# Optimization experiments

Measured on AMD Instinct MI355X. Metric: run time of the kernel, lower is better.

Reference implementation:

```python
import jax, jax.numpy as jnp
import numpy as np


def _silu(x):
    return x * jax.nn.sigmoid(x)


def _ln(x, w, b, eps=1e-5):
    mu = x.mean(-1, keepdims=True)
    xc = x - mu
    var = (xc * xc).mean(-1, keepdims=True)
    return xc * jax.lax.rsqrt(var + eps) * w + b


def _segsum(a):
    # a: (..., Q) -> (..., Q, Q) lower-triangular cumulative segment sums
    Q = a.shape[-1]
    cs = jnp.cumsum(a, axis=-1)
    ss = cs[..., :, None] - cs[..., None, :]
    mask = jnp.tril(jnp.ones((Q, Q), dtype=bool))
    return jnp.where(mask, ss, -jnp.inf)


def _ssd(x, A, Bm, Cm, chunk=64):
    # Mamba2 SSD dual (chunked) form. x:(b,l,h,p) pre-scaled by dt, A:(b,l,h)=dt*A, Bm/Cm:(b,l,n)
    b, l, h, p = x.shape
    c = l // chunk
    x = x.reshape(b, c, chunk, h, p)
    A = A.reshape(b, c, chunk, h).transpose(0, 3, 1, 2)          # (b,h,c,q)
    Bm = Bm.reshape(b, c, chunk, -1)
    Cm = Cm.reshape(b, c, chunk, -1)
    Acs = jnp.cumsum(A, axis=-1)                                  # (b,h,c,q)
    Lmat = jnp.exp(_segsum(A))                                    # (b,h,c,q,q)
    Yd = jnp.einsum('bcln,bcsn,bhcls,bcshp->bclhp', Cm, Bm, Lmat, x)
    dec = jnp.exp(Acs[..., -1:] - Acs)                            # (b,h,c,q)
    states = jnp.einsum('bcln,bhcl,bclhp->bchpn', Bm, dec, x)     # (b,c,h,p,n)
    cdec = jnp.exp(Acs[..., -1]).transpose(2, 0, 1)               # (c,b,h)
    st = states.transpose(1, 0, 2, 3, 4)                          # (c,b,h,p,n)

    def step(carry, inp):
        s, d = inp
        return carry * d[..., None, None] + s, carry

    _, prev = jax.lax.scan(step, jnp.zeros_like(st[0]), (st, cdec))
    prev = prev.transpose(1, 0, 2, 3, 4)                          # (b,c,h,p,n)
    Yo = jnp.einsum('bcln,bchpn,bhcl->bclhp', Cm, prev, jnp.exp(Acs))
    return (Yd + Yo).reshape(b, l, h, p)


def _mamba(x, in_w, in_b, conv_w, conv_b, A_log, D, dt_bias, rms_w, out_w, headdim, d_state):
    b, l, _ = x.shape
    nh = A_log.shape[0]
    di = nh * headdim
    zxbcdt = x @ in_w.T + in_b
    z = zxbcdt[..., :di]
    xBC = zxbcdt[..., di:2 * di + 2 * d_state]
    dt = jax.nn.softplus(zxbcdt[..., -nh:] + dt_bias)             # (b,l,nh)
    K = conv_w.shape[-1]
    xp = jnp.pad(xBC, ((0, 0), (K - 1, 0), (0, 0)))               # causal depthwise conv
    xBC = sum(xp[:, k:k + l, :] * conv_w[:, k] for k in range(K))
    xBC = _silu(xBC + conv_b)
    xs = xBC[..., :di].reshape(b, l, nh, headdim)
    Bm = xBC[..., di:di + d_state]
    Cm = xBC[..., di + d_state:]
    A = -jnp.exp(A_log)
    y = _ssd(xs * dt[..., None], dt * A, Bm, Cm)
    y = y + D[None, None, :, None] * xs
    y = y.reshape(b, l, di) * _silu(z)                            # gated RMSNorm
    y = y * jax.lax.rsqrt(jnp.mean(y * y, -1, keepdims=True) + 1e-5) * rms_w
    return y @ out_w.T


def setup_inputs() -> dict:
    key = jax.random.key(0)
    ks = iter(jax.random.split(key, 64))

    def nrm(shape, s):
        return jax.random.normal(next(ks), shape, jnp.float32) * s

    d = {}
    d['x'] = jax.random.normal(next(ks), (4, 128, 64, 64), jnp.float32)
    d['seed_tok_w'] = nrm((8, 128), 0.08)
    d['seed_tok_b'] = jnp.zeros((8,), jnp.float32)
    d['seed_detok_w'] = nrm((128, 8), 0.3)
    d['seed_detok_b'] = jnp.zeros((128,), jnp.float32)
    d['sm_in_w'] = nrm((66, 8), 0.3)
    d['sm_in_b'] = jnp.zeros((66,), jnp.float32)
    d['sm_conv_w'] = nrm((48, 3), 0.3)
    d['sm_conv_b'] = jnp.zeros((48,), jnp.float32)
    d['sm_A_log'] = jnp.log(jnp.arange(1, 3, dtype=jnp.float32))
    d['sm_D'] = jnp.ones((2,), jnp.float32)
    d['sm_dt_bias'] = jnp.full((2,), -4.0, jnp.float32)
    d['sm_rms_w'] = jnp.ones((16,), jnp.float32)
    d['sm_out_w'] = nrm((8, 16), 0.2)
    d['cm_in_w'] = nrm((2, 196, 16), 0.2)
    d['cm_in_b'] = jnp.zeros((2, 196), jnp.float32)
    d['cm_conv_w'] = nrm((2, 160, 3), 0.3)
    d['cm_conv_b'] = jnp.zeros((2, 160), jnp.float32)
    d['cm_A_log'] = jnp.tile(jnp.log(jnp.arange(1, 5, dtype=jnp.float32)), (2, 1))
    d['cm_D'] = jnp.ones((2, 4), jnp.float32)
    d['cm_dt_bias'] = jnp.full((2, 4), -4.0, jnp.float32)
    d['cm_rms_w'] = jnp.ones((2, 32), jnp.float32)
    d['cm_out_w'] = nrm((2, 16, 32), 0.15)
    d['cross_W'] = jnp.eye(8, dtype=jnp.float32) + 0.01 * jax.random.normal(next(ks), (8, 8), jnp.float32)
    d['norm1_w'] = jnp.ones((128,), jnp.float32)
    d['norm1_b'] = jnp.zeros((128,), jnp.float32)
    d['norm2_w'] = jnp.ones((128,), jnp.float32)
    d['norm2_b'] = jnp.zeros((128,), jnp.float32)
    d['fc1_w'] = nrm((256, 128), 0.08)
    d['fc1_b'] = jnp.zeros((256,), jnp.float32)
    d['dw_w'] = nrm((256, 1, 3, 3), 0.2)
    d['dw_b'] = jnp.zeros((256,), jnp.float32)
    d['fc2_w'] = nrm((128, 256), 0.06)
    d['fc2_b'] = jnp.zeros((128,), jnp.float32)
    d['skip_scale'] = jnp.ones((1,), jnp.float32)
    return d


def reference(x, seed_tok_w, seed_tok_b, seed_detok_w, seed_detok_b,
              sm_in_w, sm_in_b, sm_conv_w, sm_conv_b, sm_A_log, sm_D, sm_dt_bias, sm_rms_w, sm_out_w,
              cm_in_w, cm_in_b, cm_conv_w, cm_conv_b, cm_A_log, cm_D, cm_dt_bias, cm_rms_w, cm_out_w,
              cross_W, norm1_w, norm1_b, norm2_w, norm2_b,
              fc1_w, fc1_b, dw_w, dw_b, fc2_w, fc2_b, skip_scale):
    B, C, H, W = x.shape
    L = H * W
    # --- GlobalSeed ---
    g = jnp.einsum('bchw,gc->bghw', x, seed_tok_w) + seed_tok_b[None, :, None, None]
    gf = g.reshape(B, -1, L).transpose(0, 2, 1)                   # (B,L,G)
    gf = _mamba(gf, sm_in_w, sm_in_b, sm_conv_w, sm_conv_b, sm_A_log, sm_D,
                sm_dt_bias, sm_rms_w, sm_out_w, 8, 16) + gf
    det = jnp.einsum('blg,cg->blc', gf, seed_detok_w) + seed_detok_b
    seed = x + det.transpose(0, 2, 1).reshape(B, C, H, W)
    # --- split-channel cascaded SSD (shared weights across splits) ---
    xn = _ln(x.reshape(B, C, L).transpose(0, 2, 1), norm1_w, norm1_b)   # (B,L,C)
    S = cross_W.shape[0]
    xs = jnp.stack(jnp.split(xn, S, axis=-1))                     # (S,B,L,C/S)

    def cascade(xi):
        for i in range(cm_in_w.shape[0]):
            xi = _mamba(xi, cm_in_w[i], cm_in_b[i], cm_conv_w[i], cm_conv_b[i],
                        cm_A_log[i], cm_D[i], cm_dt_bias[i], cm_rms_w[i], cm_out_w[i], 8, 64)
        return xi

    ys = jax.vmap(cascade)(xs) + xs * skip_scale
    # --- SubCrossToken mixing ---
    gm = ys.mean(axis=2)                                          # (S,B,Cs)
    wsm = jax.nn.softmax(cross_W, axis=1)
    gmix = jnp.einsum('qbc,qp->pbc', gm, wsm)
    ys = ys + gmix[:, :, None, :]
    out = ys.transpose(1, 2, 0, 3).reshape(B, L, -1)
    out = _ln(out, norm2_w, norm2_b)
    out = out.transpose(0, 2, 1).reshape(B, C, H, W) + seed
    # --- ConvFFN ---
    h1 = jnp.einsum('bchw,oc->bohw', out, fc1_w) + fc1_b[None, :, None, None]
    dw = jax.lax.conv_general_dilated(h1, dw_w, (1, 1), 'SAME',
                                      feature_group_count=h1.shape[1],
                                      dimension_numbers=('NCHW', 'OIHW', 'NCHW'))
    h2 = jax.nn.gelu(dw + dw_b[None, :, None, None])
    ffn = jnp.einsum('bohw,co->bchw', h2, fc2_w) + fc2_b[None, :, None, None]
    return out + ffn
```

## Files before the change

### kernel.cpp

```cpp
#include <hip/hip_runtime.h>
#include <math.h>

#define B_ 4
#define CCH 128
#define HH 64
#define WW 64
#define LL 4096
#define NCHK 64

__device__ __forceinline__ float siluf(float x) { return x / (1.f + __expf(-x)); }
__device__ __forceinline__ float softplusf(float x) { return (x > 20.f) ? x : log1pf(__expf(x)); }
__device__ __forceinline__ int swz(int n, int l) {
  return (n << 6) + ((((l >> 2) ^ ((n >> 2) & 15)) << 2) | (l & 3));
}

__global__ __launch_bounds__(256) void k_seedtok(const float* __restrict__ x,
    const float* __restrict__ w, const float* __restrict__ bias, float* __restrict__ gf)
{
  __shared__ float tile[128*65];
  __shared__ float sw[8*128];
  __shared__ float bl[8];
  int tid = threadIdx.x;
  int b = blockIdx.x >> 6;
  int l0 = (blockIdx.x & 63) << 6;
  for (int i = tid; i < 1024; i += 256) sw[i] = w[i];
  if (tid < 8) bl[tid] = bias[tid];
  for (int i = tid; i < 8192; i += 256) {
    int l = i & 63, c = i >> 6;
    tile[c*65 + l] = x[((size_t)b*CCH + c)*LL + l0 + l];
  }
  __syncthreads();
  int l = tid & 63, q = tid >> 6;
  float a0 = bl[2*q], a1 = bl[2*q+1];
  const float* w0 = &sw[(2*q)*128];
  const float* w1 = &sw[(2*q+1)*128];
#pragma unroll 4
  for (int c = 0; c < 128; ++c) {
    float xv = tile[c*65 + l];
    a0 += xv * w0[c];
    a1 += xv * w1[c];
  }
  *(float2*)&gf[((size_t)b*LL + l0 + l)*8 + 2*q] = make_float2(a0, a1);
}

template<int DIN, int NZ, int NDS, int NDT>
__global__ __launch_bounds__(256) void k_inproj(
    const float* __restrict__ src, int srcMode,
    const float* __restrict__ in_w, const float* __restrict__ in_b,
    const float* __restrict__ conv_w, const float* __restrict__ conv_b,
    const float* __restrict__ dt_bias,
    float* __restrict__ zb, float* __restrict__ dtb,
    float* __restrict__ xsb, float* __restrict__ Bb, float* __restrict__ Cb)
{
  constexpr int NXBC = NZ + 2*NDS;
  constexpr int NTOT = 2*NZ + 2*NDS + NDT;
  constexpr int NZQ  = NZ/4;
  constexpr int NDSQ = NDS/4;
  constexpr int XP   = DIN + 1;
  __shared__ float xt[66*XP];
  __shared__ float wl[NTOT*DIN];
  __shared__ float cwl[NXBC*3];
  __shared__ float cbl[NXBC];
  __shared__ float ibl[NTOT];
  __shared__ float dts[64*NDT];
  __shared__ float hp[NXBC*2];
  int tid = threadIdx.x;
  int seq = blockIdx.x >> 6;
  int l0  = (blockIdx.x & 63) << 6;
  for (int i = tid; i < NTOT*DIN; i += 256) wl[i] = in_w[i];
  for (int i = tid; i < NXBC*3; i += 256) cwl[i] = conv_w[i];
  for (int i = tid; i < NXBC; i += 256) cbl[i] = conv_b[i];
  for (int i = tid; i < NTOT; i += 256) ibl[i] = in_b[i];
  const float* sp; int sstr;
  if (srcMode == 0) { sp = src + (size_t)seq*LL*DIN; sstr = DIN; }
  else { sp = src + (size_t)(seq & 3)*LL*CCH + (seq >> 2)*16; sstr = CCH; }
  for (int i = tid; i < 66*DIN; i += 256) {
    int r = i / DIN, d = i % DIN;
    int l = l0 - 2 + r;
    xt[r*XP + d] = (l >= 0) ? sp[(size_t)l*sstr + d] : 0.f;
  }
  __syncthreads();
  for (int i = tid; i < 2*NXBC; i += 256) {
    int t = i & 1, ch = i >> 1;
    const float* wr = &wl[(NZ + ch)*DIN];
    const float* xp = &xt[t*XP];
    float acc = 0.f;
#pragma unroll
    for (int d = 0; d < DIN; ++d) acc += xp[d]*wr[d];
    hp[ch*2 + t] = acc;
  }
  __syncthreads();
  int l = tid & 63, w4 = tid >> 6;
  float xr2[DIN];
#pragma unroll
  for (int d = 0; d < DIN; ++d) xr2[d] = xt[(l+2)*XP + d];
  size_t gl = (size_t)seq*LL + l0 + l;
  int tok = l0 + l;
  float v0ok = (tok >= 2) ? 1.f : 0.f;
  float v1ok = (tok >= 1) ? 1.f : 0.f;
  {
    float zv[NZQ];
#pragma unroll
    for (int j = 0; j < NZQ; ++j) {
      int row = w4*NZQ + j;
      const float* wr = &wl[row*DIN];
      float acc = ibl[row];
#pragma unroll
      for (int d = 0; d < DIN; ++d) acc += xr2[d]*wr[d];
      zv[j] = acc;
    }
#pragma unroll
    for (int g = 0; g < NZQ/4; ++g)
      *(float4*)&zb[gl*NZ + w4*NZQ + 4*g] = make_float4(zv[4*g], zv[4*g+1], zv[4*g+2], zv[4*g+3]);
  }
  if (w4 < NDT) {
    int row = NTOT - NDT + w4;
    const float* wr = &wl[row*DIN];
    float acc = ibl[row] + dt_bias[w4];
#pragma unroll
    for (int d = 0; d < DIN; ++d) acc += xr2[d]*wr[d];
    dts[l*NDT + w4] = softplusf(acc);
  }
  auto convch = [&](int ch) -> float {
    int row = NZ + ch;
    const float* wr = &wl[row*DIN];
    float pm = 0.f;
#pragma unroll
    for (int d = 0; d < DIN; ++d) pm += xr2[d]*wr[d];
    float m1 = __shfl_up(pm, 1, 64);
    float m2 = __shfl_up(pm, 2, 64);
    float h0 = hp[ch*2 + 0], h1 = hp[ch*2 + 1];
    if (l == 0) m1 = h1;
    m2 = (l == 0) ? h0 : ((l == 1) ? h1 : m2);
    float ib = ibl[row];
    float conv = cbl[ch] + (m2+ib)*v0ok*cwl[ch*3+0] + (m1+ib)*v1ok*cwl[ch*3+1] + (pm+ib)*cwl[ch*3+2];
    return siluf(conv);
  };
  {
    float xv[NZQ];
#pragma unroll
    for (int j = 0; j < NZQ; ++j) xv[j] = convch(w4*NZQ + j);
#pragma unroll
    for (int g = 0; g < NZQ/4; ++g)
      *(float4*)&xsb[gl*NZ + w4*NZQ + 4*g] = make_float4(xv[4*g], xv[4*g+1], xv[4*g+2], xv[4*g+3]);
  }
  {
    float bv[NDSQ];
#pragma unroll
    for (int j = 0; j < NDSQ; ++j) bv[j] = convch(NZ + w4*NDSQ + j);
#pragma unroll
    for (int g = 0; g < NDSQ/4; ++g)
      *(float4*)&Bb[gl*NDS + w4*NDSQ + 4*g] = make_float4(bv[4*g], bv[4*g+1], bv[4*g+2], bv[4*g+3]);
  }
  {
    float cv[NDSQ];
#pragma unroll
    for (int j = 0; j < NDSQ; ++j) cv[j] = convch(NZ + NDS + w4*NDSQ + j);
#pragma unroll
    for (int g = 0; g < NDSQ/4; ++g)
      *(float4*)&Cb[gl*NDS + w4*NDSQ + 4*g] = make_float4(cv[4*g], cv[4*g+1], cv[4*g+2], cv[4*g+3]);
  }
  __syncthreads();
  if (tid < 64) {
    if constexpr (NDT == 4) {
      *(float4*)&dtb[((size_t)seq*LL + l0 + tid)*4] =
          make_float4(dts[tid*4], dts[tid*4+1], dts[tid*4+2], dts[tid*4+3]);
    } else {
      *(float2*)&dtb[((size_t)seq*LL + l0 + tid)*NDT] = make_float2(dts[tid*NDT], dts[tid*NDT+1]);
    }
  }
}

__global__ __launch_bounds__(256, 3) void k_inssd(
    const float* __restrict__ src, int srcMode,
    const float* __restrict__ in_w, const float* __restrict__ in_b,
    const float* __restrict__ conv_w, const float* __restrict__ conv_b,
    const float* __restrict__ dt_bias, const float* __restrict__ A_log,
    float* __restrict__ zb, float* __restrict__ xsb, float* __restrict__ Cb,
    float* __restrict__ ybuf, float* __restrict__ states,
    float* __restrict__ cdec, float* __restrict__ acsOut)
{
  const int DIN = 16, NZ = 32, NDS = 64, DI = 32;
  const int NXBC = 160, NTOT = 196;
  __shared__ float sm[12518];
  float* Bt  = sm;
  float* Ct  = sm + 4096;
  float* U   = sm + 8192;
  float* wl  = U;
  float* cwl = U + 3136;
  float* cbl = U + 3616;
  float* ibl = U + 3776;
  float* hp  = U + 3972;
  float* ha  = U + 4292;
  float* xde = U;
  int tid = threadIdx.x;
  int cid = blockIdx.x & 63;
  int seq = blockIdx.x >> 6;
  int l0  = cid << 6;
  int lane = tid & 63, w = tid >> 6;
  const float* sp; int sstr;
  if (srcMode == 0) { sp = src + (size_t)seq*LL*DIN; sstr = DIN; }
  else { sp = src + (size_t)(seq & 3)*LL*CCH + (seq >> 2)*16; sstr = CCH; }
  float xr2[DIN];
  {
    const float* p = sp + (size_t)(l0 + lane)*sstr;
#pragma unroll
    for (int k = 0; k < 4; ++k) {
      float4 v = *(const float4*)(p + 4*k);
      xr2[4*k+0]=v.x; xr2[4*k+1]=v.y; xr2[4*k+2]=v.z; xr2[4*k+3]=v.w;
    }
  }
  for (int i = tid; i < NTOT*DIN; i += 256) wl[i] = in_w[i];
  for (int i = tid; i < NXBC*3; i += 256) cwl[i] = conv_w[i];
  for (int i = tid; i < NXBC; i += 256) cbl[i] = conv_b[i];
  for (int i = tid; i < NTOT; i += 256) ibl[i] = in_b[i];
  if (tid < 32) {
    int t = tid >> 4, d = tid & 15;
    int tok = l0 - 2 + t;
    ha[t*17 + d] = (tok >= 0) ? sp[(size_t)tok*sstr + d] : 0.f;
  }
  __syncthreads();
  for (int i = tid; i < 2*NXBC; i += 256) {
    int t = i & 1, ch = i >> 1;
    const float* wr = &wl[(NZ + ch)*DIN];
    const float* hr = &ha[t*17];
    float acc = 0.f;
#pragma unroll
    for (int d = 0; d < DIN; ++d) acc += hr[d]*wr[d];
    hp[ch*2 + t] = acc;
  }
  __syncthreads();
  size_t gl = (size_t)seq*LL + l0 + lane;
  int tok = l0 + lane;
  float v0ok = (tok >= 2) ? 1.f : 0.f;
  float v1ok = (tok >= 1) ? 1.f : 0.f;
  {
    float zv[8];
#pragma unroll
    for (int j = 0; j < 8; ++j) {
      int row = w*8 + j;
      const float* wr = &wl[row*DIN];
      float acc = ibl[row];
#pragma unroll
      for (int d = 0; d < DIN; ++d) acc += xr2[d]*wr[d];
      zv[j] = acc;
    }
    *(float4*)&zb[gl*NZ + w*8 + 0] = make_float4(zv[0], zv[1], zv[2], zv[3]);
    *(float4*)&zb[gl*NZ + w*8 + 4] = make_float4(zv[4], zv[5], zv[6], zv[7]);
  }
  float dtv;
  {
    int row = NTOT - 4 + w;
    const float* wr = &wl[row*DIN];
    float acc = ibl[row] + dt_bias[w];
#pragma unroll
    for (int d = 0; d < DIN; ++d) acc += xr2[d]*wr[d];
    dtv = softplusf(acc);
  }
  auto convch = [&](int ch) -> float {
    int row = NZ + ch;
    const float* wr = &wl[row*DIN];
    float pm = 0.f;
#pragma unroll
    for (int d = 0; d < DIN; ++d) pm += xr2[d]*wr[d];
    float m1 = __shfl_up(pm, 1, 64);
    float m2 = __shfl_up(pm, 2, 64);
    float h0 = hp[ch*2 + 0], h1 = hp[ch*2 + 1];
    if (lane == 0) m1 = h1;
    m2 = (lane == 0) ? h0 : ((lane == 1) ? h1 : m2);
    float ib = ibl[row];
    float conv = cbl[ch] + (m2+ib)*v0ok*cwl[ch*3+0] + (m1+ib)*v1ok*cwl[ch*3+1] + (pm+ib)*cwl[ch*3+2];
    return siluf(conv);
  };
  float xv[8];
#pragma unroll
  for (int j = 0; j < 8; ++j) xv[j] = convch(w*8 + j);
  *(float4*)&xsb[gl*DI + w*8 + 0] = make_float4(xv[0], xv[1], xv[2], xv[3]);
  *(float4*)&xsb[gl*DI + w*8 + 4] = make_float4(xv[4], xv[5], xv[6], xv[7]);
#pragma unroll
  for (int j = 0; j < 16; ++j) {
    int n = w*16 + j;
    Bt[swz(n, lane)] = convch(NZ + n);
  }
  {
    float cv[16];
#pragma unroll
    for (int j = 0; j < 16; ++j) {
      int n = w*16 + j;
      cv[j] = convch(NZ + NDS + n);
      Ct[swz(n, lane)] = cv[j];
    }
#pragma unroll
    for (int g = 0; g < 4; ++g)
      *(float4*)&Cb[gl*NDS + w*16 + 4*g] = make_float4(cv[4*g], cv[4*g+1], cv[4*g+2], cv[4*g+3]);
  }
  __syncthreads();
  float Aval = -__expf(A_log[w]);
  float v = dtv * Aval;
#pragma unroll
  for (int off = 1; off < 64; off <<= 1) {
    float t = __shfl_up(v, off, 64);
    if (lane >= off) v += t;
  }
  float acs_l = v;
  float m = __shfl(v, 31, 64);
  float acsLast = __shfl(v, 63, 64);
  float el = __expf(fminf(acs_l - m, 60.f));
  float fl = __expf(fminf(m - acs_l, 60.f));
  {
    float s1 = dtv*fl;
    float* xe = &xde[(w*64 + lane)*8];
    *(float4*)xe     = make_float4(xv[0]*s1, xv[1]*s1, xv[2]*s1, xv[3]*s1);
    *(float4*)(xe+4) = make_float4(xv[4]*s1, xv[5]*s1, xv[6]*s1, xv[7]*s1);
  }
  int lt = (tid >> 4) << 2, st = (tid & 15) << 2;
  float acc[4][4] = {};
#pragma unroll 4
  for (int n = 0; n < 64; ++n) {
    float4 cvv = *(const float4*)&Ct[swz(n, lt)];
    float4 bvv = *(const float4*)&Bt[swz(n, st)];
    float cc[4] = {cvv.x, cvv.y, cvv.z, cvv.w};
    float bb[4] = {bvv.x, bvv.y, bvv.z, bvv.w};
#pragma unroll
    for (int i2 = 0; i2 < 4; ++i2)
#pragma unroll
      for (int j2 = 0; j2 < 4; ++j2)
        acc[i2][j2] += cc[i2]*bb[j2];
  }
  __syncthreads();
#pragma unroll
  for (int j = 0; j < 4; ++j) {
    *(float4*)&Ct[swz(st + j, lt)] = make_float4(acc[0][j], acc[1][j], acc[2][j], acc[3][j]);
  }
  __syncthreads();
  int lg = lane >> 2, lm = lane & 3;
  float ya[8] = {0,0,0,0,0,0,0,0};
#pragma unroll 4
  for (int s = 0; s < 64; ++s) {
    float g = Ct[(s << 6) + (((lg ^ ((s >> 2) & 15))) << 2 | lm)];
    g = (s <= lane) ? g : 0.f;
    const float* xr = &xde[(w*64 + s)*8];
    float4 a0 = *(const float4*)xr, a1 = *(const float4*)(xr + 4);
    ya[0] += g*a0.x; ya[1] += g*a0.y; ya[2] += g*a0.z; ya[3] += g*a0.w;
    ya[4] += g*a1.x; ya[5] += g*a1.y; ya[6] += g*a1.z; ya[7] += g*a1.w;
  }
  float* yp = &ybuf[gl*DI + w*8];
  *(float4*)yp     = make_float4(ya[0]*el, ya[1]*el, ya[2]*el, ya[3]*el);
  *(float4*)(yp+4) = make_float4(ya[4]*el, ya[5]*el, ya[6]*el, ya[7]*el);
  {
    float r2 = __expf(acsLast - m);
    float sa[8] = {0,0,0,0,0,0,0,0};
#pragma unroll 4
    for (int ll = 0; ll < 64; ++ll) {
      float b = Bt[swz(lane, ll)];
      const float* xr = &xde[(w*64 + ll)*8];
      float4 a0 = *(const float4*)xr, a1 = *(const float4*)(xr + 4);
      sa[0] += b*a0.x; sa[1] += b*a0.y; sa[2] += b*a0.z; sa[3] += b*a0.w;
      sa[4] += b*a1.x; sa[5] += b*a1.y; sa[6] += b*a1.z; sa[7] += b*a1.w;
    }
    float* sp2 = &states[(((size_t)seq*4 + w)*NCHK + cid)*(size_t)(8*NDS) + lane*8];
    *(float4*)sp2     = make_float4(sa[0]*r2, sa[1]*r2, sa[2]*r2, sa[3]*r2);
    *(float4*)(sp2+4) = make_float4(sa[4]*r2, sa[5]*r2, sa[6]*r2, sa[7]*r2);
  }
  if (lane == 63) cdec[((size_t)seq*4 + w)*NCHK + cid] = __expf(acsLast);
  acsOut[((size_t)seq*4 + w)*LL + l0 + lane] = acs_l;
}

template<int DS, int NH>
__global__ __launch_bounds__(256) void k_ssd1(
    const float* __restrict__ xs, const float* __restrict__ dtb,
    const float* __restrict__ Bb, const float* __restrict__ Cb,
    const float* __restrict__ A_log,
    float* __restrict__ ybuf, float* __restrict__ states,
    float* __restrict__ cdec, float* __restrict__ acsOut)
{
  constexpr int DI = NH*8;
  constexpr int NG = DS/4;
  __shared__ __align__(16) float BtBl[DS*64];
  __shared__ __align__(16) float CtGt[64*64];
  __shared__ __align__(16) float xde[NH*64*8];
  int tid = threadIdx.x;
  int cid = blockIdx.x & 63;
  int seq = blockIdx.x >> 6;
  int l0  = cid << 6;
  for (int i = tid; i < 16*DS; i += 256) {
    int ng = i % NG, l = i / NG;
    size_t g = ((size_t)seq*LL + l0 + l)*DS + 4*ng;
    float4 bv = *(const float4*)&Bb[g];
    float4 cv = *(const float4*)&Cb[g];
    BtBl[swz(4*ng+0, l)] = bv.x; BtBl[swz(4*ng+1, l)] = bv.y;
    BtBl[swz(4*ng+2, l)] = bv.z; BtBl[swz(4*ng+3, l)] = bv.w;
    CtGt[swz(4*ng+0, l)] = cv.x; CtGt[swz(4*ng+1, l)] = cv.y;
    CtGt[swz(4*ng+2, l)] = cv.z; CtGt[swz(4*ng+3, l)] = cv.w;
  }
  __syncthreads();
  int lt = (tid >> 4) << 2, st = (tid & 15) << 2;
  float acc[4][4] = {};
#pragma unroll 4
  for (int n = 0; n < DS; ++n) {
    float4 cv = *(const float4*)&CtGt[swz(n, lt)];
    float4 bv = *(const float4*)&BtBl[swz(n, st)];
    float cc[4] = {cv.x, cv.y, cv.z, cv.w};
    float bb[4] = {bv.x, bv.y, bv.z, bv.w};
#pragma unroll
    for (int i2 = 0; i2 < 4; ++i2)
#pragma unroll
      for (int j2 = 0; j2 < 4; ++j2)
        acc[i2][j2] += cc[i2]*bb[j2];
  }
  __syncthreads();
#pragma unroll
  for (int j = 0; j < 4; ++j) {
    float4 gv = make_float4(acc[0][j], acc[1][j], acc[2][j], acc[3][j]);
    *(float4*)&CtGt[swz(st + j, lt)] = gv;
  }
  for (int i = tid; i < 16*DS; i += 256) {
    int ng = i % NG, l = i / NG;
    float4 bv = *(const float4*)&Bb[((size_t)seq*LL + l0 + l)*DS + 4*ng];
    *(float4*)&BtBl[l*DS + 4*ng] = bv;
  }
  __syncthreads();
  int w = tid >> 6, lane = tid & 63;
  if (w < NH) {
    int h = w;
    float dt_l = dtb[((size_t)seq*LL + l0 + lane)*NH + h];
    float Aval = -__expf(A_log[h]);
    float v = dt_l * Aval;
#pragma unroll
    for (int off = 1; off < 64; off <<= 1) {
      float t = __shfl_up(v, off, 64);
      if (lane >= off) v += t;
    }
    float acs_l = v;
    float m = __shfl(v, 31, 64);
    float acsLast = __shfl(v, 63, 64);
    float el = __expf(fminf(acs_l - m, 60.f));
    float fl = __expf(fminf(m - acs_l, 60.f));
    const float* xp = &xs[((size_t)seq*LL + l0 + lane)*DI + h*8];
    float4 x0 = *(const float4*)xp, x1 = *(const float4*)(xp + 4);
    float s1 = dt_l*fl;
    float* xe = &xde[(h*64 + lane)*8];
    *(float4*)xe     = make_float4(x0.x*s1, x0.y*s1, x0.z*s1, x0.w*s1);
    *(float4*)(xe+4) = make_float4(x1.x*s1, x1.y*s1, x1.z*s1, x1.w*s1);
    int lg = lane >> 2, lm = lane & 3;
    float ya[8] = {0,0,0,0,0,0,0,0};
#pragma unroll 4
    for (int s = 0; s < 64; ++s) {
      float g = CtGt[(s << 6) + ((((lg ^ ((s >> 2) & 15))) << 2) | lm)];
      g = (s <= lane) ? g : 0.f;
      const float* xr = &xde[(h*64 + s)*8];
      float4 a0 = *(const float4*)xr, a1 = *(const float4*)(xr + 4);
      ya[0] += g*a0.x; ya[1] += g*a0.y; ya[2] += g*a0.z; ya[3] += g*a0.w;
      ya[4] += g*a1.x; ya[5] += g*a1.y; ya[6] += g*a1.z; ya[7] += g*a1.w;
    }
    float* yp = &ybuf[((size_t)seq*LL + l0 + lane)*DI + h*8];
    *(float4*)yp     = make_float4(ya[0]*el, ya[1]*el, ya[2]*el, ya[3]*el);
    *(float4*)(yp+4) = make_float4(ya[4]*el, ya[5]*el, ya[6]*el, ya[7]*el);
    if (lane < DS) {
      float r2 = __expf(acsLast - m);
      float sa[8] = {0,0,0,0,0,0,0,0};
#pragma unroll 4
      for (int ll = 0; ll < 64; ++ll) {
        float b = BtBl[ll*DS + lane];
        const float* xr = &xde[(h*64 + ll)*8];
        float4 a0 = *(const float4*)xr, a1 = *(const float4*)(xr + 4);
        sa[0] += b*a0.x; sa[1] += b*a0.y; sa[2] += b*a0.z; sa[3] += b*a0.w;
        sa[4] += b*a1.x; sa[5] += b*a1.y; sa[6] += b*a1.z; sa[7] += b*a1.w;
      }
      float* sp2 = &states[(((size_t)seq*NH + h)*NCHK + cid)*(size_t)(8*DS) + lane*8];
      *(float4*)sp2     = make_float4(sa[0]*r2, sa[1]*r2, sa[2]*r2, sa[3]*r2);
      *(float4*)(sp2+4) = make_float4(sa[4]*r2, sa[5]*r2, sa[6]*r2, sa[7]*r2);
    }
    if (lane == 63) cdec[((size_t)seq*NH + h)*NCHK + cid] = __expf(acsLast);
    acsOut[((size_t)seq*NH + h)*LL + l0 + lane] = acs_l;
  }
}

__global__ __launch_bounds__(512) void k_scan(float* __restrict__ st, const float* __restrict__ cd, int PN)
{
  int tid = threadIdx.x;
  size_t base = (size_t)blockIdx.x * NCHK * PN + tid;
  const float* c = cd + (size_t)blockIdx.x * NCHK;
  float carry = 0.f;
  for (int k = 0; k < NCHK; ++k) {
    size_t a = base + (size_t)k*PN;
    float s = st[a];
    st[a] = carry;
    carry = carry*c[k] + s;
  }
}

template<int DS, int NH>
__global__ __launch_bounds__(256) void k_ssd_yo(
    float* __restrict__ ybuf, const float* __restrict__ Cb,
    const float* __restrict__ prevSt, const float* __restrict__ acsG,
    const float* __restrict__ Dp, const float* __restrict__ xs)
{
  constexpr int DI = NH*8;
  constexpr int NG = DS/4;
  __shared__ __align__(16) float Ct2[DS*64];
  __shared__ __align__(16) float pvs[NH*DS*8];
  int tid = threadIdx.x;
  int cid = blockIdx.x & 63;
  int seq = blockIdx.x >> 6;
  int l0  = cid << 6;
  for (int i = tid; i < 16*DS; i += 256) {
    int ng = i % NG, l = i / NG;
    float4 cv = *(const float4*)&Cb[((size_t)seq*LL + l0 + l)*DS + 4*ng];
    Ct2[swz(4*ng+0, l)] = cv.x; Ct2[swz(4*ng+1, l)] = cv.y;
    Ct2[swz(4*ng+2, l)] = cv.z; Ct2[swz(4*ng+3, l)] = cv.w;
  }
  for (int i = tid; i < NH*DS*8; i += 256) {
    int h = i / (DS*8), r = i % (DS*8);
    pvs[i] = prevSt[(((size_t)seq*NH + h)*NCHK + cid)*(size_t)(DS*8) + r];
  }
  __syncthreads();
  int w = tid >> 6, lane = tid & 63;
  if (w < NH) {
    int h = w;
    float el = __expf(acsG[((size_t)seq*NH + h)*LL + l0 + lane]);
    float Dh = Dp[h];
    int lg = lane >> 2, lm = lane & 3;
    float acc[8] = {0,0,0,0,0,0,0,0};
#pragma unroll 4
    for (int n = 0; n < DS; ++n) {
      float c = Ct2[(n << 6) + ((((lg ^ ((n >> 2) & 15))) << 2) | lm)];
      const float* pr = &pvs[(h*DS + n)*8];
      float4 p0 = *(const float4*)pr, p1 = *(const float4*)(pr + 4);
      acc[0] += c*p0.x; acc[1] += c*p0.y; acc[2] += c*p0.z; acc[3] += c*p0.w;
      acc[4] += c*p1.x; acc[5] += c*p1.y; acc[6] += c*p1.z; acc[7] += c*p1.w;
    }
    size_t gi = ((size_t)seq*LL + l0 + lane)*DI + h*8;
    float4 y0 = *(const float4*)&ybuf[gi], y1 = *(const float4*)&ybuf[gi+4];
    float4 xv0 = *(const float4*)&xs[gi], xv1 = *(const float4*)&xs[gi+4];
    y0.x += el*acc[0] + Dh*xv0.x; y0.y += el*acc[1] + Dh*xv0.y;
    y0.z += el*acc[2] + Dh*xv0.z; y0.w += el*acc[3] + Dh*xv0.w;
    y1.x += el*acc[4] + Dh*xv1.x; y1.y += el*acc[5] + Dh*xv1.y;
    y1.z += el*acc[6] + Dh*xv1.z; y1.w += el*acc[7] + Dh*xv1.w;
    *(float4*)&ybuf[gi] = y0; *(float4*)&ybuf[gi+4] = y1;
  }
}

template<int DI, int DOUT>
__global__ __launch_bounds__(256) void k_gate(
    const float* __restrict__ ybuf, const float* __restrict__ zbuf,
    const float* __restrict__ rms_w, const float* __restrict__ out_w,
    float* __restrict__ dst, int resMode, const float* __restrict__ res,
    const float* __restrict__ skipPtr)
{
  __shared__ float ow[DOUT*DI];
  __shared__ float rw[DI];
  int tid = threadIdx.x;
  for (int i = tid; i < DOUT*DI; i += 256) ow[i] = out_w[i];
  for (int i = tid; i < DI; i += 256) rw[i] = rms_w[i];
  __syncthreads();
  size_t idx = (size_t)blockIdx.x*256 + tid;
  float y[DI];
  const float* yp = ybuf + idx*DI;
  const float* zp = zbuf + idx*DI;
  float ss = 0.f;
#pragma unroll
  for (int i = 0; i < DI; ++i) {
    float z = zp[i];
    float g = yp[i] * (z / (1.f + __expf(-z)));
    y[i] = g; ss += g*g;
  }
  float r = rsqrtf(ss*(1.f/DI) + 1e-5f);
#pragma unroll
  for (int i = 0; i < DI; ++i) y[i] *= r*rw[i];
  const float* rp = nullptr; float skip = 1.f;
  int seq = (int)(idx / LL), l = (int)(idx % LL);
  if (resMode == 1) rp = res + idx*DOUT;
  else if (resMode == 2) {
    int s = seq / B_, b = seq % B_;
    rp = res + ((size_t)b*LL + l)*CCH + s*DOUT;
    skip = skipPtr[0];
  }
  float* dp = dst + idx*DOUT;
#pragma unroll
  for (int o = 0; o < DOUT; ++o) {
    float acc = 0.f;
#pragma unroll
    for (int i = 0; i < DI; ++i) acc += y[i]*ow[o*DI + i];
    if (rp) acc += skip * rp[o];
    dp[o] = acc;
  }
}

__global__ __launch_bounds__(256) void k_ln1(const float* __restrict__ x,
    const float* __restrict__ w, const float* __restrict__ bb, float* __restrict__ xn)
{
  __shared__ float tile[128*65];
  __shared__ float mu[64], rs[64];
  int tid = threadIdx.x;
  int b = blockIdx.x >> 6;
  int l0 = (blockIdx.x & 63) << 6;
  for (int i = tid; i < 8192; i += 256) {
    int l = i & 63, c = i >> 6;
    tile[c*65 + l] = x[((size_t)b*CCH + c)*LL + l0 + l];
  }
  __syncthreads();
  if (tid < 64) {
    float s = 0.f;
    for (int c = 0; c < CCH; ++c) s += tile[c*65 + tid];
    float m = s * (1.f/CCH);
    float v = 0.f;
    for (int c = 0; c < CCH; ++c) { float d = tile[c*65 + tid] - m; v += d*d; }
    mu[tid] = m; rs[tid] = rsqrtf(v*(1.f/CCH) + 1e-5f);
  }
  __syncthreads();
  for (int i = tid; i < 8192; i += 256) {
    int c = i & 127, l = i >> 7;
    xn[((size_t)b*LL + l0 + l)*CCH + c] = (tile[c*65 + l] - mu[l])*rs[l]*w[c] + bb[c];
  }
}

__global__ __launch_bounds__(256) void k_gm(const float* __restrict__ ys, float* __restrict__ gm)
{
  __shared__ float red[256];
  int tid = threadIdx.x;
  int seq = blockIdx.x;
  int c = tid & 15, lane = tid >> 4;
  float s = 0.f;
  for (int l = lane; l < LL; l += 16) s += ys[((size_t)seq*LL + l)*16 + c];
  red[tid] = s;
  __syncthreads();
  if (tid < 16) {
    float t = 0.f;
    for (int g = 0; g < 16; ++g) t += red[g*16 + tid];
    gm[(size_t)seq*16 + tid] = t * (1.f/LL);
  }
}

__global__ __launch_bounds__(256) void k_mix(const float* __restrict__ gm,
    const float* __restrict__ crossW, float* __restrict__ gmix)
{
  __shared__ float wsm[64];
  int tid = threadIdx.x;
  if (tid < 8) {
    float mx = -1e30f;
    for (int p = 0; p < 8; ++p) mx = fmaxf(mx, crossW[tid*8 + p]);
    float e[8]; float s = 0.f;
    for (int p = 0; p < 8; ++p) { e[p] = __expf(crossW[tid*8 + p] - mx); s += e[p]; }
    for (int p = 0; p < 8; ++p) wsm[tid*8 + p] = e[p] / s;
  }
  __syncthreads();
  for (int i = tid; i < 512; i += 256) {
    int c = i & 15; int bb = (i >> 4) & 3; int p = i >> 6;
    float acc = 0.f;
    for (int q = 0; q < 8; ++q) acc += gm[((size_t)(q*B_ + bb))*16 + c] * wsm[q*8 + p];
    gmix[((size_t)(p*B_ + bb))*16 + c] = acc;
  }
}

__global__ __launch_bounds__(256) void k_out2(const float* __restrict__ ys,
    const float* __restrict__ gmix, const float* __restrict__ w, const float* __restrict__ bb,
    const float* __restrict__ x, const float* __restrict__ gf2,
    const float* __restrict__ dw, const float* __restrict__ db,
    float* __restrict__ outb)
{
  __shared__ float tile[128*65];
  __shared__ float mu[64], rs[64];
  int tid = threadIdx.x;
  int b = blockIdx.x >> 6;
  int l0 = (blockIdx.x & 63) << 6;
  for (int i = tid; i < 8192; i += 256) {
    int c = i & 15; int l = (i >> 4) & 63; int s = i >> 10;
    int seq = s*B_ + b;
    tile[(s*16 + c)*65 + l] = ys[((size_t)seq*LL + l0 + l)*16 + c] + gmix[(size_t)seq*16 + c];
  }
  __syncthreads();
  if (tid < 64) {
    float sm = 0.f;
    for (int c = 0; c < 128; ++c) sm += tile[c*65 + tid];
    float m = sm * (1.f/128.f);
    float v = 0.f;
    for (int c = 0; c < 128; ++c) { float d = tile[c*65 + tid] - m; v += d*d; }
    mu[tid] = m; rs[tid] = rsqrtf(v*(1.f/128.f) + 1e-5f);
  }
  __syncthreads();
  int lfix = tid & 63;
  float g8[8];
  {
    const float* gp = gf2 + ((size_t)b*LL + l0 + lfix)*8;
#pragma unroll
    for (int k = 0; k < 8; ++k) g8[k] = gp[k];
  }
  for (int i = tid; i < 8192; i += 256) {
    int l = i & 63, c = i >> 6;
    size_t gi = ((size_t)b*CCH + c)*LL + l0 + l;
    float det = db[c];
#pragma unroll
    for (int k = 0; k < 8; ++k) det += g8[k]*dw[c*8 + k];
    outb[gi] = (tile[c*65 + l] - mu[l])*rs[l]*w[c] + bb[c] + x[gi] + det;
  }
}

__global__ __launch_bounds__(256) void k_fc1(const float* __restrict__ src,
    const float* __restrict__ w, const float* __restrict__ bias, float* __restrict__ dst)
{
  constexpr int WP = 129;
  __shared__ float st[128*64];
  __shared__ float wt[64*WP];
  int tid = threadIdx.x;
  int blk = blockIdx.x;
  int ot = blk & 3;
  int lt = (blk >> 2) & 63;
  int b  = blk >> 8;
  int l0 = lt << 6, o0 = ot << 6;
  for (int i = tid; i < 8192; i += 256) {
    int l = i & 63, c = i >> 6;
    st[c*64 + l] = src[((size_t)b*CCH + c)*LL + l0 + l];
  }
  for (int i = tid; i < 8192; i += 256) {
    int c = i & 127, o = i >> 7;
    wt[o*WP + c] = w[(size_t)(o0 + o)*128 + c];
  }
  __syncthreads();
  int l4 = (tid & 15) << 2, o4 = (tid >> 4) << 2;
  float a0[4] = {}, a1[4] = {}, a2[4] = {}, a3[4] = {};
#pragma unroll 4
  for (int c = 0; c < 128; ++c) {
    float4 sv = *(float4*)&st[c*64 + l4];
    float w0 = wt[(o4+0)*WP + c];
    float w1 = wt[(o4+1)*WP + c];
    float w2 = wt[(o4+2)*WP + c];
    float w3 = wt[(o4+3)*WP + c];
    a0[0] += w0*sv.x; a0[1] += w0*sv.y; a0[2] += w0*sv.z; a0[3] += w0*sv.w;
    a1[0] += w1*sv.x; a1[1] += w1*sv.y; a1[2] += w1*sv.z; a1[3] += w1*sv.w;
    a2[0] += w2*sv.x; a2[1] += w2*sv.y; a2[2] += w2*sv.z; a2[3] += w2*sv.w;
    a3[0] += w3*sv.x; a3[1] += w3*sv.y; a3[2] += w3*sv.z; a3[3] += w3*sv.w;
  }
  float* rows[4] = {a0, a1, a2, a3};
#pragma unroll
  for (int j = 0; j < 4; ++j) {
    int o = o0 + o4 + j;
    float bi = bias[o];
    float* a = rows[j];
    *(float4*)&dst[((size_t)b*256 + o)*LL + l0 + l4] =
        make_float4(a[0]+bi, a[1]+bi, a[2]+bi, a[3]+bi);
  }
}

__global__ __launch_bounds__(256) void k_dw(const float* __restrict__ h1,
    const float* __restrict__ w, const float* __restrict__ bias, float* __restrict__ h2)
{
  __shared__ float tile[66*66];
  int tid = threadIdx.x;
  int blk = blockIdx.x;
  const float* base = h1 + (size_t)blk*LL;
  const float* wp = w + (blk & 255)*9;
  float bi = bias[blk & 255];
  for (int i = tid; i < 66*66; i += 256) {
    int r = i / 66, cc = i % 66;
    int gr = r - 1, gc = cc - 1;
    tile[i] = (gr >= 0 && gr < HH && gc >= 0 && gc < WW) ? base[gr*WW + gc] : 0.f;
  }
  float w00 = wp[0], w01 = wp[1], w02 = wp[2];
  float w10 = wp[3], w11 = wp[4], w12 = wp[5];
  float w20 = wp[6], w21 = wp[7], w22 = wp[8];
  __syncthreads();
  float* outp = h2 + (size_t)blk*LL;
#pragma unroll
  for (int k = 0; k < 16; ++k) {
    int j = tid + k*256;
    int row = j >> 6, col = j & 63;
    const float* t0 = &tile[row*66 + col];
    float acc = t0[0]*w00  + t0[1]*w01  + t0[2]*w02
              + t0[66]*w10 + t0[67]*w11 + t0[68]*w12
              + t0[132]*w20 + t0[133]*w21 + t0[134]*w22;
    float v = acc + bi;
    float u = 0.7978845608028654f*(v + 0.044715f*v*v*v);
    float e = __expf(2.f*u);
    float th = 1.f - 2.f/(e + 1.f);
    outp[j] = 0.5f*v*(1.f + th);
  }
}

__global__ __launch_bounds__(256) void k_fc2(const float* __restrict__ h2,
    const float* __restrict__ w, const float* __restrict__ bias,
    const float* __restrict__ resid, float* __restrict__ dst)
{
  constexpr int WP = 260;
  __shared__ float st[128*64];
  __shared__ float wt[32*WP];
  int tid = threadIdx.x;
  int blk = blockIdx.x;
  int ct = blk & 3;
  int lt = (blk >> 2) & 63;
  int b  = blk >> 8;
  int l0 = lt << 6, c0 = ct << 5;
  for (int i = tid; i < 32*256; i += 256) {
    int o = i & 255, c = i >> 8;
    wt[c*WP + o] = w[(size_t)(c0 + c)*256 + o];
  }
  int l4 = (tid & 15) << 2, c2 = (tid >> 4) << 1;
  float a0[4] = {}, a1[4] = {};
  for (int ko = 0; ko < 256; ko += 128) {
    __syncthreads();
    for (int i = tid; i < 8192; i += 256) {
      int l = i & 63, o = i >> 6;
      st[o*64 + l] = h2[((size_t)b*256 + ko + o)*LL + l0 + l];
    }
    __syncthreads();
#pragma unroll 4
    for (int o = 0; o < 128; ++o) {
      float4 sv = *(float4*)&st[o*64 + l4];
      float w0 = wt[(c2+0)*WP + ko + o];
      float w1 = wt[(c2+1)*WP + ko + o];
      a0[0] += w0*sv.x; a0[1] += w0*sv.y; a0[2] += w0*sv.z; a0[3] += w0*sv.w;
      a1[0] += w1*sv.x; a1[1] += w1*sv.y; a1[2] += w1*sv.z; a1[3] += w1*sv.w;
    }
  }
  float* rows[2] = {a0, a1};
#pragma unroll
  for (int j = 0; j < 2; ++j) {
    int c = c0 + c2 + j;
    float bi = bias[c];
    size_t gi = ((size_t)b*CCH + c)*LL + l0 + l4;
    float4 rv = *(const float4*)&resid[gi];
    float* a = rows[j];
    *(float4*)&dst[gi] = make_float4(a[0]+bi+rv.x, a[1]+bi+rv.y, a[2]+bi+rv.z, a[3]+bi+rv.w);
  }
}

extern "C" void kernel_launch(void* const* d_in, const int* in_sizes, int n_in,
                              void* d_out, int out_size, void* d_ws, size_t ws_size,
                              hipStream_t stream) {
  (void)in_sizes; (void)n_in; (void)out_size; (void)ws_size;
  const float* x        = (const float*)d_in[0];
  const float* tok_w    = (const float*)d_in[1];
  const float* tok_b    = (const float*)d_in[2];
  const float* detok_w  = (const float*)d_in[3];
  const float* detok_b  = (const float*)d_in[4];
  const float* sm_in_w  = (const float*)d_in[5];
  const float* sm_in_b  = (const float*)d_in[6];
  const float* sm_conv_w= (const float*)d_in[7];
  const float* sm_conv_b= (const float*)d_in[8];
  const float* sm_A_log = (const float*)d_in[9];
  const float* sm_D     = (const float*)d_in[10];
  const float* sm_dt_b  = (const float*)d_in[11];
  const float* sm_rms_w = (const float*)d_in[12];
  const float* sm_out_w = (const float*)d_in[13];
  const float* cm_in_w  = (const float*)d_in[14];
  const float* cm_in_b  = (const float*)d_in[15];
  const float* cm_conv_w= (const float*)d_in[16];
  const float* cm_conv_b= (const float*)d_in[17];
  const float* cm_A_log = (const float*)d_in[18];
  const float* cm_D     = (const float*)d_in[19];
  const float* cm_dt_b  = (const float*)d_in[20];
  const float* cm_rms_w = (const float*)d_in[21];
  const float* cm_out_w = (const float*)d_in[22];
  const float* cross_W  = (const float*)d_in[23];
  const float* n1w      = (const float*)d_in[24];
  const float* n1b      = (const float*)d_in[25];
  const float* n2w      = (const float*)d_in[26];
  const float* n2b      = (const float*)d_in[27];
  const float* fc1w     = (const float*)d_in[28];
  const float* fc1b     = (const float*)d_in[29];
  const float* dww      = (const float*)d_in[30];
  const float* dwb      = (const float*)d_in[31];
  const float* fc2w     = (const float*)d_in[32];
  const float* fc2b     = (const float*)d_in[33];
  const float* skp      = (const float*)d_in[34];
  float* ws  = (float*)d_ws;
  float* out = (float*)d_out;

  const size_t SGF0 = 0;
  const size_t SOUTn= 131072;
  const size_t XN   = 2097152;
  const size_t YS   = 4194304;
  const size_t OUTB = 6291456;
  const size_t GM   = 8388608;
  const size_t GMIX = 8389120;
  const size_t SCR  = 8389632;
  const size_t CZ   = SCR;
  const size_t CXS  = CZ   + 4194304;
  const size_t CCF  = CXS  + 4194304;
  const size_t CACS = CCF  + 8388608;
  const size_t CST  = CACS + 2097152;
  const size_t CCD  = CST  + 4194304;
  const size_t CY   = CCD  + 8192;
  const size_t XB   = CY   + 4194304;
  const size_t SZ   = SCR;
  const size_t SDT  = SZ  + 262144;
  const size_t SXS  = SDT + 32768;
  const size_t SB   = SXS + 262144;
  const size_t SC   = SB  + 262144;
  const size_t SACS = SC  + 262144;
  const size_t SST  = SACS + 32768;
  const size_t SCD  = SST + 65536;
  const size_t SY   = SCD + 512;
  const size_t H1 = SCR;
  const size_t H2 = SCR + 4194304;

  k_seedtok<<<B_*64, 256, 0, stream>>>(x, tok_w, tok_b, ws + SGF0);
  k_inproj<8,16,16,2><<<B_*64, 256, 0, stream>>>(ws + SGF0, 0, sm_in_w, sm_in_b, sm_conv_w,
      sm_conv_b, sm_dt_b, ws + SZ, ws + SDT, ws + SXS, ws + SB, ws + SC);
  k_ssd1<16,2><<<B_*NCHK, 256, 0, stream>>>(ws + SXS, ws + SDT, ws + SB, ws + SC,
      sm_A_log, ws + SY, ws + SST, ws + SCD, ws + SACS);
  k_scan<<<B_*2, 128, 0, stream>>>(ws + SST, ws + SCD, 128);
  k_ssd_yo<16,2><<<B_*NCHK, 256, 0, stream>>>(ws + SY, ws + SC, ws + SST, ws + SACS, sm_D, ws + SXS);
  k_gate<16,8><<<B_*LL/256, 256, 0, stream>>>(ws + SY, ws + SZ, sm_rms_w, sm_out_w,
      ws + SOUTn, 1, ws + SGF0, skp);

  k_ln1<<<B_*64, 256, 0, stream>>>(x, n1w, n1b, ws + XN);

  k_inssd<<<32*NCHK, 256, 0, stream>>>(ws + XN, 1, cm_in_w, cm_in_b, cm_conv_w,
      cm_conv_b, cm_dt_b, cm_A_log, ws + CZ, ws + CXS, ws + CCF,
      ws + CY, ws + CST, ws + CCD, ws + CACS);
  k_scan<<<32*4, 512, 0, stream>>>(ws + CST, ws + CCD, 512);
  k_ssd_yo<64,4><<<32*NCHK, 256, 0, stream>>>(ws + CY, ws + CCF, ws + CST, ws + CACS, cm_D, ws + CXS);
  k_gate<32,16><<<32*LL/256, 256, 0, stream>>>(ws + CY, ws + CZ, cm_rms_w, cm_out_w,
      ws + XB, 0, nullptr, skp);

  k_inssd<<<32*NCHK, 256, 0, stream>>>(ws + XB, 0, cm_in_w + 3136, cm_in_b + 196,
      cm_conv_w + 480, cm_conv_b + 160, cm_dt_b + 4, cm_A_log + 4, ws + CZ, ws + CXS, ws + CCF,
      ws + CY, ws + CST, ws + CCD, ws + CACS);
  k_scan<<<32*4, 512, 0, stream>>>(ws + CST, ws + CCD, 512);
  k_ssd_yo<64,4><<<32*NCHK, 256, 0, stream>>>(ws + CY, ws + CCF, ws + CST, ws + CACS, cm_D + 4, ws + CXS);
  k_gate<32,16><<<32*LL/256, 256, 0, stream>>>(ws + CY, ws + CZ, cm_rms_w + 32, cm_out_w + 512,
      ws + YS, 2, ws + XN, skp);

  k_gm<<<32, 256, 0, stream>>>(ws + YS, ws + GM);
  k_mix<<<1, 256, 0, stream>>>(ws + GM, cross_W, ws + GMIX);
  k_out2<<<B_*64, 256, 0, stream>>>(ws + YS, ws + GMIX, n2w, n2b,
      x, ws + SOUTn, detok_w, detok_b, ws + OUTB);

  k_fc1<<<B_*64*4, 256, 0, stream>>>(ws + OUTB, fc1w, fc1b, ws + H1);
  k_dw<<<B_*256, 256, 0, stream>>>(ws + H1, dww, dwb, ws + H2);
  k_fc2<<<B_*64*4, 256, 0, stream>>>(ws + H2, fc2w, fc2b, ws + OUTB, out);
}
```

Measured before the change: 587.7 us.

## Fuse SSD inter-chunk output with gating, RMSNorm and out-projection kernel

Merges the k_ssd_yo and k_gate kernels into one k_yogate kernel. The block computes the Yo contribution, applies the SiLU gate, stages the gated values in shared memory, reduces the RMS sum across heads, and runs the output projection with residual, with each of four waves producing a quarter of the outputs. This removes one kernel launch per mamba layer and the write and re-read of the y buffer. In exchange the block uses more shared memory, and for NH=2 half the waves sit idle during the Yo phase.

Measured after the change: 557.4 us. -5.1%, faster.

```diff
diff --git a/kernel.cpp b/kernel.cpp
--- a/kernel.cpp
+++ b/kernel.cpp
@@ -490,16 +490,26 @@
   }
 }
 
-template<int DS, int NH>
-__global__ __launch_bounds__(256) void k_ssd_yo(
-    float* __restrict__ ybuf, const float* __restrict__ Cb,
+template<int DS, int NH, int DOUT>
+__global__ __launch_bounds__(256) void k_yogate(
+    const float* __restrict__ ybuf, const float* __restrict__ Cb,
     const float* __restrict__ prevSt, const float* __restrict__ acsG,
-    const float* __restrict__ Dp, const float* __restrict__ xs)
+    const float* __restrict__ Dp, const float* __restrict__ xs,
+    const float* __restrict__ zb,
+    const float* __restrict__ rms_w, const float* __restrict__ out_w,
+    float* __restrict__ dst, int resMode, const float* __restrict__ res,
+    const float* __restrict__ skipPtr)
 {
   constexpr int DI = NH*8;
   constexpr int NG = DS/4;
+  constexpr int DIP = DI + 4;
+  constexpr int OQ = DOUT/4;
   __shared__ __align__(16) float Ct2[DS*64];
   __shared__ __align__(16) float pvs[NH*DS*8];
+  __shared__ __align__(16) float gt[64*DIP];
+  __shared__ float ps[NH*64];
+  __shared__ float ow[DOUT*DI];
+  __shared__ float rwl[DI];
   int tid = threadIdx.x;
   int cid = blockIdx.x & 63;
   int seq = blockIdx.x >> 6;
@@ -514,77 +524,81 @@
     int h = i / (DS*8), r = i % (DS*8);
     pvs[i] = prevSt[(((size_t)seq*NH + h)*NCHK + cid)*(size_t)(DS*8) + r];
   }
+  for (int i = tid; i < DOUT*DI; i += 256) ow[i] = out_w[i];
+  for (int i = tid; i < DI; i += 256) rwl[i] = rms_w[i];
   __syncthreads();
   int w = tid >> 6, lane = tid & 63;
   if (w < NH) {
-    int h = w;
-    float el = __expf(acsG[((size_t)seq*NH + h)*LL + l0 + lane]);
-    float Dh = Dp[h];
+    float el = __expf(acsG[((size_t)seq*NH + w)*LL + l0 + lane]);
+    float Dh = Dp[w];
     int lg = lane >> 2, lm = lane & 3;
     float acc[8] = {0,0,0,0,0,0,0,0};
 #pragma unroll 4
     for (int n = 0; n < DS; ++n) {
       float c = Ct2[(n << 6) + ((((lg ^ ((n >> 2) & 15))) << 2) | lm)];
-      const float* pr = &pvs[(h*DS + n)*8];
+      const float* pr = &pvs[(w*DS + n)*8];
       float4 p0 = *(const float4*)pr, p1 = *(const float4*)(pr + 4);
       acc[0] += c*p0.x; acc[1] += c*p0.y; acc[2] += c*p0.z; acc[3] += c*p0.w;
       acc[4] += c*p1.x; acc[5] += c*p1.y; acc[6] += c*p1.z; acc[7] += c*p1.w;
     }
-    size_t gi = ((size_t)seq*LL + l0 + lane)*DI + h*8;
+    size_t gi = ((size_t)seq*LL + l0 + lane)*DI + w*8;
     float4 y0 = *(const float4*)&ybuf[gi], y1 = *(const float4*)&ybuf[gi+4];
     float4 xv0 = *(const float4*)&xs[gi], xv1 = *(const float4*)&xs[gi+4];
-    y0.x += el*acc[0] + Dh*xv0.x; y0.y += el*acc[1] + Dh*xv0.y;
-    y0.z += el*acc[2] + Dh*xv0.z; y0.w += el*acc[3] + Dh*xv0.w;
-    y1.x += el*acc[4] + Dh*xv1.x; y1.y += el*acc[5] + Dh*xv1.y;
-    y1.z += el*acc[6] + Dh*xv1.z; y1.w += el*acc[7] + Dh*xv1.w;
-    *(float4*)&ybuf[gi] = y0; *(float4*)&ybuf[gi+4] = y1;
-  }
-}
-
-template<int DI, int DOUT>
-__global__ __launch_bounds__(256) void k_gate(
-    const float* __restrict__ ybuf, const float* __restrict__ zbuf,
-    const float* __restrict__ rms_w, const float* __restrict__ out_w,
-    float* __restrict__ dst, int resMode, const float* __restrict__ res,
-    const float* __restrict__ skipPtr)
-{
-  __shared__ float ow[DOUT*DI];
-  __shared__ float rw[DI];
-  int tid = threadIdx.x;
-  for (int i = tid; i < DOUT*DI; i += 256) ow[i] = out_w[i];
-  for (int i = tid; i < DI; i += 256) rw[i] = rms_w[i];
-  __syncthreads();
-  size_t idx = (size_t)blockIdx.x*256 + tid;
-  float y[DI];
-  const float* yp = ybuf + idx*DI;
-  const float* zp = zbuf + idx*DI;
-  float ss = 0.f;
-#pragma unroll
-  for (int i = 0; i < DI; ++i) {
-    float z = zp[i];
-    float g = yp[i] * (z / (1.f + __expf(-z)));
-    y[i] = g; ss += g*g;
-  }
-  float r = rsqrtf(ss*(1.f/DI) + 1e-5f);
-#pragma unroll
-  for (int i = 0; i < DI; ++i) y[i] *= r*rw[i];
+    float4 z0 = *(const float4*)&zb[gi], z1 = *(const float4*)&zb[gi+4];
+    float g[8];
+    g[0] = (y0.x + el*acc[0] + Dh*xv0.x) * siluf(z0.x);
+    g[1] = (y0.y + el*acc[1] + Dh*xv0.y) * siluf(z0.y);
+    g[2] = (y0.z + el*acc[2] + Dh*xv0.z) * siluf(z0.z);
+    g[3] = (y0.w + el*acc[3] + Dh*xv0.w) * siluf(z0.w);
+    g[4] = (y1.x + el*acc[4] + Dh*xv1.x) * siluf(z1.x);
+    g[5] = (y1.y + el*acc[5] + Dh*xv1.y) * siluf(z1.y);
+    g[6] = (y1.z + el*acc[6] + Dh*xv1.z) * siluf(z1.z);
+    g[7] = (y1.w + el*acc[7] + Dh*xv1.w) * siluf(z1.w);
+    float ssum = 0.f;
+#pragma unroll
+    for (int j = 0; j < 8; ++j) ssum += g[j]*g[j];
+    float* gp = &gt[lane*DIP + w*8];
+    *(float4*)gp     = make_float4(g[0], g[1], g[2], g[3]);
+    *(float4*)(gp+4) = make_float4(g[4], g[5], g[6], g[7]);
+    ps[w*64 + lane] = ssum;
+  }
+  __syncthreads();
+  int tok = tid & 63, q = tid >> 6;
+  float rsum = 0.f;
+#pragma unroll
+  for (int h = 0; h < NH; ++h) rsum += ps[h*64 + tok];
+  float r = rsqrtf(rsum*(1.f/DI) + 1e-5f);
+  float gr[DI];
+#pragma unroll
+  for (int k = 0; k < DI/4; ++k) {
+    float4 v = *(const float4*)&gt[tok*DIP + 4*k];
+    gr[4*k+0] = v.x*r*rwl[4*k+0];
+    gr[4*k+1] = v.y*r*rwl[4*k+1];
+    gr[4*k+2] = v.z*r*rwl[4*k+2];
+    gr[4*k+3] = v.w*r*rwl[4*k+3];
+  }
+  int l = l0 + tok;
   const float* rp = nullptr; float skip = 1.f;
-  int seq = (int)(idx / LL), l = (int)(idx % LL);
-  if (resMode == 1) rp = res + idx*DOUT;
+  if (resMode == 1) rp = res + ((size_t)seq*LL + l)*DOUT + q*OQ;
   else if (resMode == 2) {
     int s = seq / B_, b = seq % B_;
-    rp = res + ((size_t)b*LL + l)*CCH + s*DOUT;
+    rp = res + ((size_t)b*LL + l)*CCH + s*DOUT + q*OQ;
     skip = skipPtr[0];
   }
-  float* dp = dst + idx*DOUT;
-#pragma unroll
-  for (int o = 0; o < DOUT; ++o) {
-    float acc = 0.f;
-#pragma unroll
-    for (int i = 0; i < DI; ++i) acc += y[i]*ow[o*DI + i];
-    if (rp) acc += skip * rp[o];
-    dp[o] = acc;
-  }
+  float ov[OQ];
+#pragma unroll
+  for (int j = 0; j < OQ; ++j) {
+    int o = q*OQ + j;
+    const float* wr = &ow[o*DI];
+    float acc2 = 0.f;
+#pragma unroll
+    for (int i = 0; i < DI; ++i) acc2 += gr[i]*wr[i];
+    if (rp) acc2 += skip * rp[j];
+    ov[j] = acc2;
+  }
+  float* dp = &dst[((size_t)seq*LL + l)*DOUT + q*OQ];
+  if constexpr (OQ == 4) *(float4*)dp = make_float4(ov[0], ov[1], ov[2], ov[3]);
+  else *(float2*)dp = make_float2(ov[0], ov[1]);
 }
 
 __global__ __launch_bounds__(256) void k_ln1(const float* __restrict__ x,
@@ -900,9 +914,8 @@
   k_ssd1<16,2><<<B_*NCHK, 256, 0, stream>>>(ws + SXS, ws + SDT, ws + SB, ws + SC,
       sm_A_log, ws + SY, ws + SST, ws + SCD, ws + SACS);
   k_scan<<<B_*2, 128, 0, stream>>>(ws + SST, ws + SCD, 128);
-  k_ssd_yo<16,2><<<B_*NCHK, 256, 0, stream>>>(ws + SY, ws + SC, ws + SST, ws + SACS, sm_D, ws + SXS);
-  k_gate<16,8><<<B_*LL/256, 256, 0, stream>>>(ws + SY, ws + SZ, sm_rms_w, sm_out_w,
-      ws + SOUTn, 1, ws + SGF0, skp);
+  k_yogate<16,2,8><<<B_*NCHK, 256, 0, stream>>>(ws + SY, ws + SC, ws + SST, ws + SACS,
+      sm_D, ws + SXS, ws + SZ, sm_rms_w, sm_out_w, ws + SOUTn, 1, ws + SGF0, skp);
 
   k_ln1<<<B_*64, 256, 0, stream>>>(x, n1w, n1b, ws + XN);
 
@@ -910,17 +923,15 @@
       cm_conv_b, cm_dt_b, cm_A_log, ws + CZ, ws + CXS, ws + CCF,
       ws + CY, ws + CST, ws + CCD, ws + CACS);
   k_scan<<<32*4, 512, 0, stream>>>(ws + CST, ws + CCD, 512);
-  k_ssd_yo<64,4><<<32*NCHK, 256, 0, stream>>>(ws + CY, ws + CCF, ws + CST, ws + CACS, cm_D, ws + CXS);
-  k_gate<32,16><<<32*LL/256, 256, 0, stream>>>(ws + CY, ws + CZ, cm_rms_w, cm_out_w,
-      ws + XB, 0, nullptr, skp);
+  k_yogate<64,4,16><<<32*NCHK, 256, 0, stream>>>(ws + CY, ws + CCF, ws + CST, ws + CACS,
+      cm_D, ws + CXS, ws + CZ, cm_rms_w, cm_out_w, ws + XB, 0, nullptr, skp);
 
   k_inssd<<<32*NCHK, 256, 0, stream>>>(ws + XB, 0, cm_in_w + 3136, cm_in_b + 196,
       cm_conv_w + 480, cm_conv_b + 160, cm_dt_b + 4, cm_A_log + 4, ws + CZ, ws + CXS, ws + CCF,
       ws + CY, ws + CST, ws + CCD, ws + CACS);
   k_scan<<<32*4, 512, 0, stream>>>(ws + CST, ws + CCD, 512);
-  k_ssd_yo<64,4><<<32*NCHK, 256, 0, stream>>>(ws + CY, ws + CCF, ws + CST, ws + CACS, cm_D + 4, ws + CXS);
-  k_gate<32,16><<<32*LL/256, 256, 0, stream>>>(ws + CY, ws + CZ, cm_rms_w + 32, cm_out_w + 512,
-      ws + YS, 2, ws + XN, skp);
+  k_yogate<64,4,16><<<32*NCHK, 256, 0, stream>>>(ws + CY, ws + CCF, ws + CST, ws + CACS,
+      cm_D + 4, ws + CXS, ws + CZ, cm_rms_w + 32, cm_out_w + 512, ws + YS, 2, ws + XN, skp);
 
   k_gm<<<32, 256, 0, stream>>>(ws + YS, ws + GM);
   k_mix<<<1, 256, 0, stream>>>(ws + GM, cross_W, ws + GMIX);
```
